# Optimization experiments

Hardware: AMD Instinct MI355X
Metric: run time of the kernel (lower is better)

## Reference

```python
import jax, jax.numpy as jnp
import numpy as np

B, S, D, H, KP, DK = 4, 2048, 1024, 16, 8, 3
DD = D // H
NEG = -1.0e9


def dense(x, W, b):
    return x @ W + b


def dw_conv_causal(x, w, b):
    # x: [B,S,D], w: [DK,D] per-channel kernel, b: [D]; left pad DK-1 zeros -> VALID conv
    xp = jnp.pad(x, ((0, 0), (DK - 1, 0), (0, 0)))
    y = b
    for t in range(DK):
        y = y + xp[:, t:t + S, :] * w[t]
    return y


def split_heads(x):
    return x.reshape(B, S, H, DD).transpose(0, 2, 1, 3)  # [B,H,S,DD]


def pool_causal(x):
    # left pad KP-1 zeros along seq, avg_pool window=stride=KP, VALID
    xp = jnp.pad(x, ((0, 0), (0, 0), (KP - 1, 0), (0, 0)))
    n = (S - 1) // KP + 1  # TF VALID output length
    return xp[:, :, :n * KP, :].reshape(B, H, n, KP, DD).mean(axis=3)


def forward(q, k, v, Wq, bq, Wk, bk, Wv, bv, Wup, bup, Wc, bc,
            wcq, bcq, wck, bck, wcv, bcv):
    norm = float(DD) ** -0.25
    qh = dense(q, Wq, bq) * norm
    kh = dense(k, Wk, bk) * norm
    vh = dense(v, Wv, bv)
    q_in = split_heads(dw_conv_causal(qh, wcq, bcq))
    k_in = split_heads(dw_conv_causal(kh, wck, bck))
    v_in = split_heads(dw_conv_causal(vh, wcv, bcv))
    qp = pool_causal(q_in)  # [B,H,n,DD]
    kp = pool_causal(k_in)
    vp = pool_causal(v_in)
    n = qp.shape[2]
    mask = NEG * (1.0 - jnp.tril(jnp.ones((n, n), dtype=qp.dtype)))
    logits = jnp.einsum('bhnd,bhmd->bhnm', qp, kp) + mask
    attn = jax.nn.softmax(logits, axis=-1)
    out = jnp.einsum('bhnm,bhmd->bhnd', attn, vp)  # [B,H,n,DD]
    up = jnp.repeat(out, KP, axis=2)[:, :, :S, :]  # upsample + crop
    up = dense(up, Wup, bup)
    merged = up.transpose(0, 2, 1, 3).reshape(B, S, D)
    return dense(merged, Wc, bc)


def setup_inputs() -> dict:
    key = jax.random.key(0)
    ks = jax.random.split(key, 20)
    w = lambda i, shp: jax.random.normal(ks[i], shp, dtype=jnp.float32) * 0.02
    return {
        'q': jax.random.normal(ks[0], (B, S, D), dtype=jnp.float32),
        'k': jax.random.normal(ks[1], (B, S, D), dtype=jnp.float32),
        'v': jax.random.normal(ks[2], (B, S, D), dtype=jnp.float32),
        'Wq': w(3, (D, D)), 'bq': jnp.zeros((D,), jnp.float32),
        'Wk': w(4, (D, D)), 'bk': jnp.zeros((D,), jnp.float32),
        'Wv': w(5, (D, D)), 'bv': jnp.zeros((D,), jnp.float32),
        'Wup': w(6, (DD, DD)), 'bup': jnp.zeros((DD,), jnp.float32),
        'Wc': w(7, (D, D)), 'bc': jnp.zeros((D,), jnp.float32),
        'wcq': w(8, (DK, D)), 'bcq': jnp.zeros((D,), jnp.float32),
        'wck': w(9, (DK, D)), 'bck': jnp.zeros((D,), jnp.float32),
        'wcv': w(10, (DK, D)), 'bcv': jnp.zeros((D,), jnp.float32),
    }


def reference(q, k, v, Wq, bq, Wk, bk, Wv, bv, Wup, bup, Wc, bc,
              wcq, bcq, wck, bck, wcv, bcv):
    return forward(q, k, v, Wq, bq, Wk, bk, Wv, bv, Wup, bup, Wc, bc,
                   wcq, bcq, wck, bck, wcv, bcv)
```

## Files before the change

### kernel.cpp

```cpp
#include <hip/hip_runtime.h>
#include <cstdint>
#include <cstddef>

#define Bc  4
#define Sc  2048
#define Dc  1024
#define Hc  16
#define DDc 64
#define Nc  256

typedef unsigned short u16;
typedef unsigned int   u32;
typedef __bf16 bf16_t;
typedef bf16_t bf16x8 __attribute__((ext_vector_type(8)));
typedef float  f32x4  __attribute__((ext_vector_type(4)));

__device__ __forceinline__ u16 f2bf(float x) {
    u32 u = __float_as_uint(x);
    return (u16)((u + 0x7FFFu + ((u >> 16) & 1u)) >> 16);
}
__device__ __forceinline__ u32 pack2(float a, float b) {
    return (u32)f2bf(a) | ((u32)f2bf(b) << 16);
}
__device__ __forceinline__ uint2 pack4(float4 x) {
    return make_uint2(pack2(x.x, x.y), pack2(x.z, x.w));
}
__device__ __forceinline__ float bf2f(u16 x) {
    return __uint_as_float((u32)x << 16);
}
__device__ __forceinline__ float4 f4add(float4 a, float4 b) {
    return make_float4(a.x + b.x, a.y + b.y, a.z + b.z, a.w + b.w);
}

__device__ __forceinline__ void gload_lds16(const void* gp, void* lp) {
    __builtin_amdgcn_global_load_lds(
        reinterpret_cast<const __attribute__((address_space(1))) void*>(
            reinterpret_cast<uintptr_t>(gp)),
        reinterpret_cast<__attribute__((address_space(3))) void*>(
            reinterpret_cast<uintptr_t>(lp)),
        16, 0, 0);
}

__global__ __launch_bounds__(256) void cast_wt4_kernel(
    const float* __restrict__ Wq, const float* __restrict__ Wk,
    const float* __restrict__ Wv, const float* __restrict__ Wc,
    u16* __restrict__ Wt4)
{
    __shared__ float T[64][65];
    const int z = blockIdx.z;
    const float* W = (z == 0) ? Wq : (z == 1) ? Wk : (z == 2) ? Wv : Wc;
    u16* Wt = Wt4 + ((size_t)z << 20);
    const int k0 = blockIdx.y * 64, n0 = blockIdx.x * 64;
    const int c = threadIdx.x & 63, r4 = threadIdx.x >> 6;
    #pragma unroll
    for (int i = 0; i < 16; ++i) {
        int r = i * 4 + r4;
        T[r][c] = W[(size_t)(k0 + r) * 1024 + n0 + c];
    }
    __syncthreads();
    #pragma unroll
    for (int i = 0; i < 16; ++i) {
        int r = i * 4 + r4;
        Wt[(size_t)(n0 + r) * 1024 + k0 + c] = f2bf(T[c][r]);
    }
}

__global__ __launch_bounds__(256) void stage_kernel(
    const float* __restrict__ q, const float* __restrict__ k,
    const float* __restrict__ v, u16* __restrict__ R)
{
    int gid = blockIdx.x * 256 + threadIdx.x;
    int c4 = gid & 255, t = (gid >> 8) & 255, b = (gid >> 16) & 3, inp = gid >> 18;
    const float* src = (inp == 0) ? q : (inp == 1) ? k : v;
    const float4* Xb = (const float4*)(src + (size_t)b * Sc * Dc) + c4;
    const float4* Xr = Xb + ((ptrdiff_t)(t << 3) - 1) * 256;

    float4 r[8];
    if (t > 0) {
        #pragma unroll
        for (int i = 0; i < 8; ++i) r[i] = Xr[(ptrdiff_t)i * 256];
    } else {
        r[0] = make_float4(0.f, 0.f, 0.f, 0.f);
        #pragma unroll
        for (int i = 1; i < 8; ++i) r[i] = Xr[(ptrdiff_t)i * 256];
    }

    float4 s8 = f4add(f4add(f4add(r[0], r[1]), f4add(r[2], r[3])),
                      f4add(f4add(r[4], r[5]), f4add(r[6], r[7])));

    size_t s0 = ((size_t)(inp * 3) << 20) + (((u32)(b * 256 + t)) << 10) + c4 * 4;
    *(uint2*)(R + s0 + (1u << 20)) = pack4(r[0]);
    *(uint2*)(R + s0 + (2u << 20)) = pack4(r[1]);
    if (t < 255) *(uint2*)(R + s0 + 1024) = pack4(s8);
    if (t == 0)  *(uint2*)(R + s0) = make_uint2(0u, 0u);
}

__global__ __launch_bounds__(256) void gemm_sec(
    u16* __restrict__ Rall, const u16* __restrict__ Wt4)
{
    __shared__ __align__(16) u16 As[128 * 32];
    __shared__ __align__(16) u16 Bs[128 * 32];

    const int tid  = threadIdx.x;
    const int lane = tid & 63;
    const int wv   = tid >> 6;
    const int z    = blockIdx.z;
    const int inp  = z / 3;
    const int m0   = blockIdx.y * 128;
    const int n0   = blockIdx.x * 128;

    const char* Ab = (const char*)(Rall + ((size_t)z << 20));
    const char* Bb = (const char*)(Wt4 + ((size_t)inp << 20));

    const int wm   = (wv & 1) * 64;
    const int wn   = (wv >> 1) * 64;
    const int mi   = lane & 15;
    const int quad = lane >> 4;

    f32x4 acc[4][4];
    #pragma unroll
    for (int i = 0; i < 4; ++i)
        #pragma unroll
        for (int j = 0; j < 4; ++j)
            acc[i][j] = (f32x4){0.f, 0.f, 0.f, 0.f};

    const int ra0 = tid >> 2, cb = (tid & 3) * 16;
    char* AsB = (char*)As;
    char* BsB = (char*)Bs;

    for (int k0 = 0; k0 < 1024; k0 += 32) {
        const size_t kb = (size_t)k0 * 2;
        gload_lds16(Ab + ((size_t)(m0 + ra0)      << 11) + kb + cb, AsB + wv * 1024);
        gload_lds16(Ab + ((size_t)(m0 + 64 + ra0) << 11) + kb + cb, AsB + 4096 + wv * 1024);
        gload_lds16(Bb + ((size_t)(n0 + ra0)      << 11) + kb + cb, BsB + wv * 1024);
        gload_lds16(Bb + ((size_t)(n0 + 64 + ra0) << 11) + kb + cb, BsB + 4096 + wv * 1024);
        __syncthreads();

        bf16x8 af[4], bfr[4];
        #pragma unroll
        for (int i = 0; i < 4; ++i)
            af[i] = *reinterpret_cast<const bf16x8*>(&As[(wm + i * 16 + mi) * 32 + quad * 8]);
        #pragma unroll
        for (int j = 0; j < 4; ++j)
            bfr[j] = *reinterpret_cast<const bf16x8*>(&Bs[(wn + j * 16 + mi) * 32 + quad * 8]);

        #pragma unroll
        for (int i = 0; i < 4; ++i)
            #pragma unroll
            for (int j = 0; j < 4; ++j)
                acc[i][j] = __builtin_amdgcn_mfma_f32_16x16x32_bf16(af[i], bfr[j], acc[i][j], 0, 0, 0);

        __syncthreads();
    }

    u16* Cs = Rall + ((size_t)z << 20);
    #pragma unroll
    for (int j = 0; j < 4; ++j) {
        const int col = n0 + wn + j * 16 + mi;
        #pragma unroll
        for (int i = 0; i < 4; ++i) {
            const int row = m0 + wm + i * 16 + quad * 4;
            #pragma unroll
            for (int r = 0; r < 4; ++r)
                Cs[(size_t)(row + r) * 1024 + col] = f2bf(acc[i][j][r]);
        }
    }
}

__global__ __launch_bounds__(256) void combine_kernel(
    const u16* __restrict__ Y,
    const float* __restrict__ wcq, const float* __restrict__ wck, const float* __restrict__ wcv,
    const float* __restrict__ bcq, const float* __restrict__ bck, const float* __restrict__ bcv,
    const float* __restrict__ bq,  const float* __restrict__ bk,  const float* __restrict__ bv,
    u16* __restrict__ qb, u16* __restrict__ kb, u16* __restrict__ vt)
{
    int gid = blockIdx.x * 256 + threadIdx.x;
    int c = gid & 1023, t = (gid >> 10) & 255, b = (gid >> 18) & 3, inp = gid >> 20;
    const float* wc = (inp == 0) ? wcq : (inp == 1) ? wck : wcv;
    const float* bconv = (inp == 0) ? bcq : (inp == 1) ? bck : bcv;
    const float* bl = (inp == 0) ? bq : (inp == 1) ? bk : bv;
    const float nrm = (inp == 2) ? 1.0f : 0.35355339059327373f;

    float w0 = wc[c], w1 = wc[1024 + c], w2 = wc[2048 + c];
    float sumw = w0 + w1 + w2, w12 = w1 + w2;

    u32 lo = gid & 0xFFFFFu;
    size_t z0 = (size_t)(inp * 3) << 20;
    float Y0  = bf2f(Y[z0 + lo]);
    float Y1  = bf2f(Y[z0 + (1u << 20) + lo]);
    float Y2  = bf2f(Y[z0 + (2u << 20) + lo]);
    float Y1p = (t > 0) ? bf2f(Y[z0 + (1u << 20) + lo - 1024]) : 0.f;
    float Y2p = (t > 0) ? bf2f(Y[z0 + (2u << 20) + lo - 1024]) : 0.f;

    float data = sumw * Y0 + w12 * (Y1 - Y1p) + w2 * (Y2 - Y2p);

    float cnt = (t == 0) ? 1.f : 8.f;
    float n0  = (t == 0) ? 0.f : ((t == 1) ? 7.f : 8.f);
    float n1  = (t == 0) ? 0.f : 8.f;
    float n2  = (t == 0) ? 1.f : 8.f;
    float val = 0.125f * (cnt * bconv[c] + nrm * (bl[c] * (n0 * w0 + n1 * w1 + n2 * w2) + data));

    int h = c >> 6, d = c & 63;
    int bh = b * 16 + h;
    u16 bfv = f2bf(val);
    if (inp == 0)
        qb[(((size_t)bh * 256 + t) << 6) + d] = bfv;
    else if (inp == 1)
        kb[(((size_t)bh * 256 + t) << 6) + d] = bfv;
    else
        vt[(size_t)bh * 80 * 256 + (size_t)d * 256 + t] = bfv;
}

__global__ __launch_bounds__(256) void vpad_kernel(u16* __restrict__ vt)
{
    const int bh = blockIdx.x;
    const int tid = threadIdx.x;
    const int rr = tid >> 4;
    const int c0 = (tid & 15) * 16;
    u32 fill = (rr == 0) ? 0x3F803F80u : 0u;
    uint4 val = make_uint4(fill, fill, fill, fill);
    uint4* p = (uint4*)(vt + (size_t)bh * 80 * 256 + (size_t)(64 + rr) * 256 + c0);
    p[0] = val;
    p[1] = val;
}

__global__ __launch_bounds__(256) void attn_mfma(
    const u16* __restrict__ qb, const u16* __restrict__ kb,
    const u16* __restrict__ vt, float* __restrict__ ao)
{
    __shared__ __align__(16) u16 Ps[4][64 * 72];
    const int bh   = blockIdx.x;
    const int tid  = threadIdx.x;
    const int wv   = tid >> 6;
    const int lane = tid & 63;
    const int mi   = lane & 15;
    const int quad = lane >> 4;

    const u16* Qb = qb + (((size_t)bh * 256 + wv * 64) << 6);
    const u16* Kb = kb + ((size_t)bh << 14);
    const u16* Vt = vt + (size_t)bh * 80 * 256;
    u16* P = Ps[wv];

    bf16x8 qf[4][2];
    #pragma unroll
    for (int it = 0; it < 4; ++it)
        #pragma unroll
        for (int kc = 0; kc < 2; ++kc)
            qf[it][kc] = *(const bf16x8*)(Qb + ((it * 16 + mi) << 6) + kc * 32 + quad * 8);

    f32x4 o[4][5];
    #pragma unroll
    for (int it = 0; it < 4; ++it)
        #pragma unroll
        for (int jn = 0; jn < 5; ++jn)
            o[it][jn] = (f32x4){0.f, 0.f, 0.f, 0.f};

    for (int kt = 0; kt <= wv; ++kt) {
        bf16x8 kf[4][2];
        #pragma unroll
        for (int jt = 0; jt < 4; ++jt)
            #pragma unroll
            for (int kc = 0; kc < 2; ++kc)
                kf[jt][kc] = *(const bf16x8*)(Kb + ((kt * 64 + jt * 16 + mi) << 6) + kc * 32 + quad * 8);

        f32x4 s[4][4];
        #pragma unroll
        for (int it = 0; it < 4; ++it)
            #pragma unroll
            for (int jt = 0; jt < 4; ++jt)
                s[it][jt] = (f32x4){0.f, 0.f, 0.f, 0.f};
        #pragma unroll
        for (int kc = 0; kc < 2; ++kc)
            #pragma unroll
            for (int it = 0; it < 4; ++it)
                #pragma unroll
                for (int jt = 0; jt < 4; ++jt)
                    s[it][jt] = __builtin_amdgcn_mfma_f32_16x16x32_bf16(qf[it][kc], kf[jt][kc], s[it][jt], 0, 0, 0);

        const bool diag = (kt == wv);
        #pragma unroll
        for (int it = 0; it < 4; ++it)
            #pragma unroll
            for (int jt = 0; jt < 4; ++jt)
                #pragma unroll
                for (int r = 0; r < 4; ++r) {
                    int qrow = it * 16 + quad * 4 + r;
                    int kcol = jt * 16 + mi;
                    float e = __expf(s[it][jt][r]);
                    if (diag && kcol > qrow) e = 0.f;
                    P[qrow * 72 + kcol] = f2bf(e);
                }

        bf16x8 pf[4][2];
        #pragma unroll
        for (int it = 0; it < 4; ++it)
            #pragma unroll
            for (int kc = 0; kc < 2; ++kc)
                pf[it][kc] = *(const bf16x8*)(P + (it * 16 + mi) * 72 + kc * 32 + quad * 8);

        bf16x8 vf[5][2];
        #pragma unroll
        for (int jn = 0; jn < 5; ++jn)
            #pragma unroll
            for (int kc = 0; kc < 2; ++kc)
                vf[jn][kc] = *(const bf16x8*)(Vt + (size_t)(jn * 16 + mi) * 256 + kt * 64 + kc * 32 + quad * 8);

        #pragma unroll
        for (int kc = 0; kc < 2; ++kc)
            #pragma unroll
            for (int it = 0; it < 4; ++it)
                #pragma unroll
                for (int jn = 0; jn < 5; ++jn)
                    o[it][jn] = __builtin_amdgcn_mfma_f32_16x16x32_bf16(pf[it][kc], vf[jn][kc], o[it][jn], 0, 0, 0);
    }

    #pragma unroll
    for (int it = 0; it < 4; ++it) {
        float inv[4];
        #pragma unroll
        for (int r = 0; r < 4; ++r) {
            float lv = __shfl(o[it][4][r], (lane & 48));
            inv[r] = 1.0f / lv;
        }
        #pragma unroll
        for (int jn = 0; jn < 4; ++jn)
            #pragma unroll
            for (int r = 0; r < 4; ++r) {
                int row = wv * 64 + it * 16 + quad * 4 + r;
                ao[(((size_t)bh * 256 + row) << 6) + jn * 16 + mi] = o[it][jn][r] * inv[r];
            }
    }
}

__global__ __launch_bounds__(256) void updense_kernel(
    const float* __restrict__ ao, const float* __restrict__ Wup,
    const float* __restrict__ bup, u16* __restrict__ ms)
{
    __shared__ float Ws[64 * 64];
    __shared__ float rows[4 * 64];
    const int tid = threadIdx.x;

    #pragma unroll
    for (int i = 0; i < 4; ++i)
        ((float4*)Ws)[tid + 256 * i] = ((const float4*)Wup)[tid + 256 * i];
    rows[tid] = ao[(size_t)blockIdx.x * 256 + tid];
    __syncthreads();

    const int r = tid >> 6, dp = tid & 63;
    const int R = blockIdx.x * 4 + r;
    const int b = R >> 12;
    const int h = (R >> 8) & 15;
    const int m = R & 255;

    float acc = bup[dp];
    #pragma unroll
    for (int d = 0; d < 64; ++d)
        acc += rows[r * 64 + d] * Ws[d * 64 + dp];

    ms[((size_t)(b * Nc + m) << 10) + h * 64 + dp] = f2bf(acc);
}

__global__ __launch_bounds__(256) void gemm_out(
    const u16* __restrict__ A, const u16* __restrict__ Bt,
    const float* __restrict__ bias, float* __restrict__ C)
{
    __shared__ __align__(16) u16 As[64 * 32];
    __shared__ __align__(16) u16 Bs[64 * 32];

    const int tid  = threadIdx.x;
    const int lane = tid & 63;
    const int wv   = tid >> 6;
    const int m0   = blockIdx.y * 64;
    const int n0   = blockIdx.x * 64;

    const int wm   = (wv >> 1) * 32;
    const int wn   = (wv & 1) * 32;
    const int mi   = lane & 15;
    const int quad = lane >> 4;

    f32x4 acc[2][2];
    #pragma unroll
    for (int i = 0; i < 2; ++i)
        #pragma unroll
        for (int j = 0; j < 2; ++j)
            acc[i][j] = (f32x4){0.f, 0.f, 0.f, 0.f};

    const char* Ab = (const char*)A;
    const char* Bb = (const char*)Bt;
    const int ra0 = tid >> 2, cb = (tid & 3) * 16;
    char* AsB = (char*)As;
    char* BsB = (char*)Bs;

    for (int k0 = 0; k0 < 1024; k0 += 32) {
        const size_t kb = (size_t)k0 * 2;
        gload_lds16(Ab + ((size_t)(m0 + ra0) << 11) + kb + cb, AsB + wv * 1024);
        gload_lds16(Bb + ((size_t)(n0 + ra0) << 11) + kb + cb, BsB + wv * 1024);
        __syncthreads();

        bf16x8 af[2], bfr[2];
        #pragma unroll
        for (int i = 0; i < 2; ++i)
            af[i] = *reinterpret_cast<const bf16x8*>(&As[(wm + i * 16 + mi) * 32 + quad * 8]);
        #pragma unroll
        for (int j = 0; j < 2; ++j)
            bfr[j] = *reinterpret_cast<const bf16x8*>(&Bs[(wn + j * 16 + mi) * 32 + quad * 8]);

        #pragma unroll
        for (int i = 0; i < 2; ++i)
            #pragma unroll
            for (int j = 0; j < 2; ++j)
                acc[i][j] = __builtin_amdgcn_mfma_f32_16x16x32_bf16(af[i], bfr[j], acc[i][j], 0, 0, 0);

        __syncthreads();
    }

    #pragma unroll
    for (int j = 0; j < 2; ++j) {
        const int col = n0 + wn + j * 16 + mi;
        const float bv = bias[col];
        #pragma unroll
        for (int i = 0; i < 2; ++i) {
            const int row = m0 + wm + i * 16 + quad * 4;
            #pragma unroll
            for (int r = 0; r < 4; ++r)
                C[(size_t)(row + r) * 1024 + col] = acc[i][j][r] + bv;
        }
    }
}

__global__ __launch_bounds__(256) void upsample_kernel(
    const float* __restrict__ C, float* __restrict__ out)
{
    const float4* C4  = (const float4*)C;
    float4*       out4 = (float4*)out;
    int idx0 = blockIdx.x * 1024 + threadIdx.x;
    #pragma unroll
    for (int rep = 0; rep < 4; ++rep) {
        int o4   = idx0 + rep * 256;
        int col4 = o4 & 255;
        int rowo = o4 >> 8;
        int b    = rowo >> 11;
        int tc   = (rowo & 2047) >> 3;
        out4[o4] = C4[(size_t)((b << 8) + tc) * 256 + col4];
    }
}

extern "C" void kernel_launch(void* const* d_in, const int* in_sizes, int n_in,
                              void* d_out, int out_size, void* d_ws, size_t ws_size,
                              hipStream_t stream) {
    const float* q   = (const float*)d_in[0];
    const float* k   = (const float*)d_in[1];
    const float* v   = (const float*)d_in[2];
    const float* Wq  = (const float*)d_in[3];
    const float* bq  = (const float*)d_in[4];
    const float* Wk  = (const float*)d_in[5];
    const float* bk  = (const float*)d_in[6];
    const float* Wv  = (const float*)d_in[7];
    const float* bv  = (const float*)d_in[8];
    const float* Wup = (const float*)d_in[9];
    const float* bup = (const float*)d_in[10];
    const float* Wc  = (const float*)d_in[11];
    const float* bc  = (const float*)d_in[12];
    const float* wcq = (const float*)d_in[13];
    const float* bcq = (const float*)d_in[14];
    const float* wck = (const float*)d_in[15];
    const float* bck = (const float*)d_in[16];
    const float* wcv = (const float*)d_in[17];
    const float* bcv = (const float*)d_in[18];

    u16* Rall = (u16*)d_out;

    char* wsb = (char*)d_ws;
    u16*   Wt4 = (u16*)wsb;
    u16*   qb  = (u16*)(wsb + 8388608);
    u16*   kb  = (u16*)(wsb + 10485760);
    u16*   vt  = (u16*)(wsb + 12582912);
    float* ao  = (float*)(wsb + 15204352);
    u16*   ms  = (u16*)(wsb + 19398656);
    float* Cf  = ao;

    cast_wt4_kernel<<<dim3(16, 16, 4), 256, 0, stream>>>(Wq, Wk, Wv, Wc, Wt4);
    stage_kernel<<<3072, 256, 0, stream>>>(q, k, v, Rall);
    gemm_sec<<<dim3(8, 8, 9), 256, 0, stream>>>(Rall, Wt4);
    combine_kernel<<<12288, 256, 0, stream>>>(Rall, wcq, wck, wcv, bcq, bck, bcv,
                                              bq, bk, bv, qb, kb, vt);
    vpad_kernel<<<64, 256, 0, stream>>>(vt);
    attn_mfma<<<64, 256, 0, stream>>>(qb, kb, vt, ao);
    updense_kernel<<<(Bc * Hc * Nc) / 4, 256, 0, stream>>>(ao, Wup, bup, ms);
    gemm_out<<<dim3(16, 16), 256, 0, stream>>>(ms, Wt4 + ((size_t)3 << 20), bc, Cf);
    upsample_kernel<<<2048, 256, 0, stream>>>(Cf, (float*)d_out);
}
```

Baseline: 276.4 us.

## Fold depthwise conv into QKV weights and fuse combine into K=3072 GEMM

Folds the causal depthwise-conv weights and the pooling scale into three scaled copies of each projection weight, so that one GEMM with K=3072 over staged pooled-sum and difference features produces pooled q/k/v directly. Bias terms are precomputed per position class. This replaces the nine separate GEMMs and the elementwise combine kernel, whose bf16 round trip through memory is removed. The attention kernel is also split into one 64-thread block per query tile instead of four waves per block, which raises block count but leaves causal tiles imbalanced across blocks. Staging reads ten rows per output instead of eight, and the larger weight workspace adds traffic in the prep kernel.

```diff
diff --git a/kernel.cpp b/kernel.cpp
--- a/kernel.cpp
+++ b/kernel.cpp
@@ -30,6 +30,9 @@
 }
 __device__ __forceinline__ float4 f4add(float4 a, float4 b) {
     return make_float4(a.x + b.x, a.y + b.y, a.z + b.z, a.w + b.w);
+}
+__device__ __forceinline__ float4 f4sub(float4 a, float4 b) {
+    return make_float4(a.x - b.x, a.y - b.y, a.z - b.z, a.w - b.w);
 }
 
 __device__ __forceinline__ void gload_lds16(const void* gp, void* lp) {
@@ -41,15 +44,16 @@
         16, 0, 0);
 }
 
-__global__ __launch_bounds__(256) void cast_wt4_kernel(
+__global__ __launch_bounds__(256) void prep_wt3(
     const float* __restrict__ Wq, const float* __restrict__ Wk,
     const float* __restrict__ Wv, const float* __restrict__ Wc,
-    u16* __restrict__ Wt4)
+    const float* __restrict__ wcq, const float* __restrict__ wck,
+    const float* __restrict__ wcv,
+    u16* __restrict__ Wt3, u16* __restrict__ Wtc)
 {
     __shared__ float T[64][65];
     const int z = blockIdx.z;
     const float* W = (z == 0) ? Wq : (z == 1) ? Wk : (z == 2) ? Wv : Wc;
-    u16* Wt = Wt4 + ((size_t)z << 20);
     const int k0 = blockIdx.y * 64, n0 = blockIdx.x * 64;
     const int c = threadIdx.x & 63, r4 = threadIdx.x >> 6;
     #pragma unroll
@@ -58,68 +62,112 @@
         T[r][c] = W[(size_t)(k0 + r) * 1024 + n0 + c];
     }
     __syncthreads();
-    #pragma unroll
-    for (int i = 0; i < 16; ++i) {
-        int r = i * 4 + r4;
-        Wt[(size_t)(n0 + r) * 1024 + k0 + c] = f2bf(T[c][r]);
-    }
+    if (z < 3) {
+        const float* wc = (z == 0) ? wcq : (z == 1) ? wck : wcv;
+        const float fs = 0.125f * ((z == 2) ? 1.0f : 0.35355339059327373f);
+        u16* dst0 = Wt3 + (size_t)z * 3145728;
+        #pragma unroll
+        for (int i = 0; i < 16; ++i) {
+            int r = i * 4 + r4;
+            int n = n0 + r;
+            float w0 = wc[n], w1 = wc[1024 + n], w2 = wc[2048 + n];
+            float s2 = fs * w2, s1 = s2 + fs * w1, s0 = s1 + fs * w0;
+            float x = T[c][r];
+            u16* dst = dst0 + (size_t)n * 3072 + k0 + c;
+            dst[0]    = f2bf(x * s0);
+            dst[1024] = f2bf(x * s1);
+            dst[2048] = f2bf(x * s2);
+        }
+    } else {
+        #pragma unroll
+        for (int i = 0; i < 16; ++i) {
+            int r = i * 4 + r4;
+            Wtc[(size_t)(n0 + r) * 1024 + k0 + c] = f2bf(T[c][r]);
+        }
+    }
+}
+
+__global__ __launch_bounds__(256) void prep_bias(
+    const float* __restrict__ wcq, const float* __restrict__ wck, const float* __restrict__ wcv,
+    const float* __restrict__ bcq, const float* __restrict__ bck, const float* __restrict__ bcv,
+    const float* __restrict__ bq,  const float* __restrict__ bk,  const float* __restrict__ bv,
+    float* __restrict__ biasT)
+{
+    int gid = blockIdx.x * 256 + threadIdx.x;
+    int c = gid & 1023, z = gid >> 10;
+    const float* wc    = (z == 0) ? wcq : (z == 1) ? wck : wcv;
+    const float* bconv = (z == 0) ? bcq : (z == 1) ? bck : bcv;
+    const float* bl    = (z == 0) ? bq  : (z == 1) ? bk  : bv;
+    const float nrm = (z == 2) ? 1.0f : 0.35355339059327373f;
+    float w0 = wc[c], w1 = wc[1024 + c], w2 = wc[2048 + c];
+    float bc_ = bconv[c], bl_ = bl[c];
+    float* dst = biasT + (size_t)z * 3072 + c;
+    dst[0]    = 0.125f * (bc_ + nrm * bl_ * w2);
+    dst[1024] = 0.125f * (8.f * bc_ + nrm * bl_ * (7.f * w0 + 8.f * w1 + 8.f * w2));
+    dst[2048] = 0.125f * (8.f * bc_ + nrm * bl_ * 8.f * (w0 + w1 + w2));
 }
 
 __global__ __launch_bounds__(256) void stage_kernel(
     const float* __restrict__ q, const float* __restrict__ k,
-    const float* __restrict__ v, u16* __restrict__ R)
+    const float* __restrict__ v, u16* __restrict__ A3)
 {
     int gid = blockIdx.x * 256 + threadIdx.x;
     int c4 = gid & 255, t = (gid >> 8) & 255, b = (gid >> 16) & 3, inp = gid >> 18;
     const float* src = (inp == 0) ? q : (inp == 1) ? k : v;
     const float4* Xb = (const float4*)(src + (size_t)b * Sc * Dc) + c4;
-    const float4* Xr = Xb + ((ptrdiff_t)(t << 3) - 1) * 256;
-
-    float4 r[8];
-    if (t > 0) {
-        #pragma unroll
-        for (int i = 0; i < 8; ++i) r[i] = Xr[(ptrdiff_t)i * 256];
+    const float4* Xr = Xb + ((ptrdiff_t)(t << 3) - 9) * 256;
+
+    float4 r[10];
+    if (t >= 2) {
+        #pragma unroll
+        for (int i = 0; i < 10; ++i) r[i] = Xr[(ptrdiff_t)i * 256];
+    } else if (t == 1) {
+        r[0] = make_float4(0.f, 0.f, 0.f, 0.f);
+        #pragma unroll
+        for (int i = 1; i < 10; ++i) r[i] = Xr[(ptrdiff_t)i * 256];
     } else {
-        r[0] = make_float4(0.f, 0.f, 0.f, 0.f);
-        #pragma unroll
-        for (int i = 1; i < 8; ++i) r[i] = Xr[(ptrdiff_t)i * 256];
-    }
-
-    float4 s8 = f4add(f4add(f4add(r[0], r[1]), f4add(r[2], r[3])),
+        #pragma unroll
+        for (int i = 0; i < 9; ++i) r[i] = make_float4(0.f, 0.f, 0.f, 0.f);
+        r[9] = Xr[(ptrdiff_t)9 * 256];
+    }
+
+    float4 A0 = f4add(f4add(f4add(r[0], r[1]), f4add(r[2], r[3])),
                       f4add(f4add(r[4], r[5]), f4add(r[6], r[7])));
-
-    size_t s0 = ((size_t)(inp * 3) << 20) + (((u32)(b * 256 + t)) << 10) + c4 * 4;
-    *(uint2*)(R + s0 + (1u << 20)) = pack4(r[0]);
-    *(uint2*)(R + s0 + (2u << 20)) = pack4(r[1]);
-    if (t < 255) *(uint2*)(R + s0 + 1024) = pack4(s8);
-    if (t == 0)  *(uint2*)(R + s0) = make_uint2(0u, 0u);
-}
-
-__global__ __launch_bounds__(256) void gemm_sec(
-    u16* __restrict__ Rall, const u16* __restrict__ Wt4)
-{
-    __shared__ __align__(16) u16 As[128 * 32];
+    float4 B1 = f4sub(r[8], r[0]);
+    float4 B2 = f4sub(r[9], r[1]);
+
+    size_t s0 = (size_t)inp * 3145728 + (size_t)(b * 256 + t) * 3072 + c4 * 4;
+    *(uint2*)(A3 + s0)        = pack4(A0);
+    *(uint2*)(A3 + s0 + 1024) = pack4(B1);
+    *(uint2*)(A3 + s0 + 2048) = pack4(B2);
+}
+
+__global__ __launch_bounds__(256) void gemm_qkv(
+    const u16* __restrict__ A3, const u16* __restrict__ Wt3,
+    const float* __restrict__ biasT,
+    u16* __restrict__ qb, u16* __restrict__ kb, u16* __restrict__ vt)
+{
+    __shared__ __align__(16) u16 As[64 * 32];
     __shared__ __align__(16) u16 Bs[128 * 32];
 
     const int tid  = threadIdx.x;
     const int lane = tid & 63;
     const int wv   = tid >> 6;
     const int z    = blockIdx.z;
-    const int inp  = z / 3;
-    const int m0   = blockIdx.y * 128;
+    const int m0   = blockIdx.y * 64;
     const int n0   = blockIdx.x * 128;
 
-    const char* Ab = (const char*)(Rall + ((size_t)z << 20));
-    const char* Bb = (const char*)(Wt4 + ((size_t)inp << 20));
-
-    const int wm   = (wv & 1) * 64;
+    const int wm   = (wv & 1) * 32;
     const int wn   = (wv >> 1) * 64;
     const int mi   = lane & 15;
     const int quad = lane >> 4;
 
-    f32x4 acc[4][4];
-    #pragma unroll
-    for (int i = 0; i < 4; ++i)
+    const char* Ab = (const char*)(A3  + (size_t)z * 3145728);
+    const char* Bb = (const char*)(Wt3 + (size_t)z * 3145728);
+
+    f32x4 acc[2][4];
+    #pragma unroll
+    for (int i = 0; i < 2; ++i)
         #pragma unroll
         for (int j = 0; j < 4; ++j)
             acc[i][j] = (f32x4){0.f, 0.f, 0.f, 0.f};
@@ -128,24 +176,23 @@
     char* AsB = (char*)As;
     char* BsB = (char*)Bs;
 
-    for (int k0 = 0; k0 < 1024; k0 += 32) {
+    for (int k0 = 0; k0 < 3072; k0 += 32) {
         const size_t kb = (size_t)k0 * 2;
-        gload_lds16(Ab + ((size_t)(m0 + ra0)      << 11) + kb + cb, AsB + wv * 1024);
-        gload_lds16(Ab + ((size_t)(m0 + 64 + ra0) << 11) + kb + cb, AsB + 4096 + wv * 1024);
-        gload_lds16(Bb + ((size_t)(n0 + ra0)      << 11) + kb + cb, BsB + wv * 1024);
-        gload_lds16(Bb + ((size_t)(n0 + 64 + ra0) << 11) + kb + cb, BsB + 4096 + wv * 1024);
+        gload_lds16(Ab + (size_t)(m0 + ra0)      * 6144 + kb + cb, AsB + wv * 1024);
+        gload_lds16(Bb + (size_t)(n0 + ra0)      * 6144 + kb + cb, BsB + wv * 1024);
+        gload_lds16(Bb + (size_t)(n0 + 64 + ra0) * 6144 + kb + cb, BsB + 4096 + wv * 1024);
         __syncthreads();
 
-        bf16x8 af[4], bfr[4];
-        #pragma unroll
-        for (int i = 0; i < 4; ++i)
+        bf16x8 af[2], bfr[4];
+        #pragma unroll
+        for (int i = 0; i < 2; ++i)
             af[i] = *reinterpret_cast<const bf16x8*>(&As[(wm + i * 16 + mi) * 32 + quad * 8]);
         #pragma unroll
         for (int j = 0; j < 4; ++j)
             bfr[j] = *reinterpret_cast<const bf16x8*>(&Bs[(wn + j * 16 + mi) * 32 + quad * 8]);
 
         #pragma unroll
-        for (int i = 0; i < 4; ++i)
+        for (int i = 0; i < 2; ++i)
             #pragma unroll
             for (int j = 0; j < 4; ++j)
                 acc[i][j] = __builtin_amdgcn_mfma_f32_16x16x32_bf16(af[i], bfr[j], acc[i][j], 0, 0, 0);
@@ -153,62 +200,47 @@
         __syncthreads();
     }
 
-    u16* Cs = Rall + ((size_t)z << 20);
-    #pragma unroll
-    for (int j = 0; j < 4; ++j) {
-        const int col = n0 + wn + j * 16 + mi;
-        #pragma unroll
-        for (int i = 0; i < 4; ++i) {
-            const int row = m0 + wm + i * 16 + quad * 4;
-            #pragma unroll
-            for (int r = 0; r < 4; ++r)
-                Cs[(size_t)(row + r) * 1024 + col] = f2bf(acc[i][j][r]);
+    const float* bT = biasT + (size_t)z * 3072;
+    if (z == 2) {
+        #pragma unroll
+        for (int j = 0; j < 4; ++j) {
+            const int col = n0 + wn + j * 16 + mi;
+            const int h = col >> 6, d = col & 63;
+            #pragma unroll
+            for (int i = 0; i < 2; ++i) {
+                const int row = m0 + wm + i * 16 + quad * 4;
+                const int b = row >> 8, t0 = row & 255;
+                const int bh = b * 16 + h;
+                u16 w[4];
+                #pragma unroll
+                for (int r = 0; r < 4; ++r) {
+                    int t = t0 + r;
+                    w[r] = f2bf(acc[i][j][r] + bT[(t < 2 ? t : 2) * 1024 + col]);
+                }
+                *(uint2*)(vt + (size_t)bh * 20480 + (size_t)d * 256 + t0) =
+                    make_uint2((u32)w[0] | ((u32)w[1] << 16), (u32)w[2] | ((u32)w[3] << 16));
+            }
         }
-    }
-}
-
-__global__ __launch_bounds__(256) void combine_kernel(
-    const u16* __restrict__ Y,
-    const float* __restrict__ wcq, const float* __restrict__ wck, const float* __restrict__ wcv,
-    const float* __restrict__ bcq, const float* __restrict__ bck, const float* __restrict__ bcv,
-    const float* __restrict__ bq,  const float* __restrict__ bk,  const float* __restrict__ bv,
-    u16* __restrict__ qb, u16* __restrict__ kb, u16* __restrict__ vt)
-{
-    int gid = blockIdx.x * 256 + threadIdx.x;
-    int c = gid & 1023, t = (gid >> 10) & 255, b = (gid >> 18) & 3, inp = gid >> 20;
-    const float* wc = (inp == 0) ? wcq : (inp == 1) ? wck : wcv;
-    const float* bconv = (inp == 0) ? bcq : (inp == 1) ? bck : bcv;
-    const float* bl = (inp == 0) ? bq : (inp == 1) ? bk : bv;
-    const float nrm = (inp == 2) ? 1.0f : 0.35355339059327373f;
-
-    float w0 = wc[c], w1 = wc[1024 + c], w2 = wc[2048 + c];
-    float sumw = w0 + w1 + w2, w12 = w1 + w2;
-
-    u32 lo = gid & 0xFFFFFu;
-    size_t z0 = (size_t)(inp * 3) << 20;
-    float Y0  = bf2f(Y[z0 + lo]);
-    float Y1  = bf2f(Y[z0 + (1u << 20) + lo]);
-    float Y2  = bf2f(Y[z0 + (2u << 20) + lo]);
-    float Y1p = (t > 0) ? bf2f(Y[z0 + (1u << 20) + lo - 1024]) : 0.f;
-    float Y2p = (t > 0) ? bf2f(Y[z0 + (2u << 20) + lo - 1024]) : 0.f;
-
-    float data = sumw * Y0 + w12 * (Y1 - Y1p) + w2 * (Y2 - Y2p);
-
-    float cnt = (t == 0) ? 1.f : 8.f;
-    float n0  = (t == 0) ? 0.f : ((t == 1) ? 7.f : 8.f);
-    float n1  = (t == 0) ? 0.f : 8.f;
-    float n2  = (t == 0) ? 1.f : 8.f;
-    float val = 0.125f * (cnt * bconv[c] + nrm * (bl[c] * (n0 * w0 + n1 * w1 + n2 * w2) + data));
-
-    int h = c >> 6, d = c & 63;
-    int bh = b * 16 + h;
-    u16 bfv = f2bf(val);
-    if (inp == 0)
-        qb[(((size_t)bh * 256 + t) << 6) + d] = bfv;
-    else if (inp == 1)
-        kb[(((size_t)bh * 256 + t) << 6) + d] = bfv;
-    else
-        vt[(size_t)bh * 80 * 256 + (size_t)d * 256 + t] = bfv;
+    } else {
+        u16* dst = z ? kb : qb;
+        #pragma unroll
+        for (int j = 0; j < 4; ++j) {
+            const int col = n0 + wn + j * 16 + mi;
+            const int h = col >> 6, d = col & 63;
+            #pragma unroll
+            for (int i = 0; i < 2; ++i) {
+                const int row = m0 + wm + i * 16 + quad * 4;
+                const int b = row >> 8;
+                const int bh = b * 16 + h;
+                #pragma unroll
+                for (int r = 0; r < 4; ++r) {
+                    int t = (row & 255) + r;
+                    dst[(((size_t)bh * 256 + t) << 6) + d] =
+                        f2bf(acc[i][j][r] + bT[(t < 2 ? t : 2) * 1024 + col]);
+                }
+            }
+        }
+    }
 }
 
 __global__ __launch_bounds__(256) void vpad_kernel(u16* __restrict__ vt)
@@ -224,22 +256,20 @@
     p[1] = val;
 }
 
-__global__ __launch_bounds__(256) void attn_mfma(
+__global__ __launch_bounds__(64) void attn_mfma(
     const u16* __restrict__ qb, const u16* __restrict__ kb,
     const u16* __restrict__ vt, float* __restrict__ ao)
 {
-    __shared__ __align__(16) u16 Ps[4][64 * 72];
-    const int bh   = blockIdx.x;
-    const int tid  = threadIdx.x;
-    const int wv   = tid >> 6;
-    const int lane = tid & 63;
+    __shared__ __align__(16) u16 P[64 * 72];
+    const int qt   = blockIdx.x;
+    const int bh   = blockIdx.y;
+    const int lane = threadIdx.x;
     const int mi   = lane & 15;
     const int quad = lane >> 4;
 
-    const u16* Qb = qb + (((size_t)bh * 256 + wv * 64) << 6);
+    const u16* Qb = qb + (((size_t)bh * 256 + qt * 64) << 6);
     const u16* Kb = kb + ((size_t)bh << 14);
     const u16* Vt = vt + (size_t)bh * 80 * 256;
-    u16* P = Ps[wv];
 
     bf16x8 qf[4][2];
     #pragma unroll
@@ -255,7 +285,7 @@
         for (int jn = 0; jn < 5; ++jn)
             o[it][jn] = (f32x4){0.f, 0.f, 0.f, 0.f};
 
-    for (int kt = 0; kt <= wv; ++kt) {
+    for (int kt = 0; kt <= qt; ++kt) {
         bf16x8 kf[4][2];
         #pragma unroll
         for (int jt = 0; jt < 4; ++jt)
@@ -277,7 +307,7 @@
                 for (int jt = 0; jt < 4; ++jt)
                     s[it][jt] = __builtin_amdgcn_mfma_f32_16x16x32_bf16(qf[it][kc], kf[jt][kc], s[it][jt], 0, 0, 0);
 
-        const bool diag = (kt == wv);
+        const bool diag = (kt == qt);
         #pragma unroll
         for (int it = 0; it < 4; ++it)
             #pragma unroll
@@ -326,7 +356,7 @@
         for (int jn = 0; jn < 4; ++jn)
             #pragma unroll
             for (int r = 0; r < 4; ++r) {
-                int row = wv * 64 + it * 16 + quad * 4 + r;
+                int row = qt * 64 + it * 16 + quad * 4 + r;
                 ao[(((size_t)bh * 256 + row) << 6) + jn * 16 + mi] = o[it][jn][r] * inv[r];
             }
     }
@@ -468,25 +498,26 @@
     const float* wcv = (const float*)d_in[17];
     const float* bcv = (const float*)d_in[18];
 
-    u16* Rall = (u16*)d_out;
+    u16* A3 = (u16*)d_out;
 
     char* wsb = (char*)d_ws;
-    u16*   Wt4 = (u16*)wsb;
-    u16*   qb  = (u16*)(wsb + 8388608);
-    u16*   kb  = (u16*)(wsb + 10485760);
-    u16*   vt  = (u16*)(wsb + 12582912);
-    float* ao  = (float*)(wsb + 15204352);
-    u16*   ms  = (u16*)(wsb + 19398656);
-    float* Cf  = ao;
-
-    cast_wt4_kernel<<<dim3(16, 16, 4), 256, 0, stream>>>(Wq, Wk, Wv, Wc, Wt4);
-    stage_kernel<<<3072, 256, 0, stream>>>(q, k, v, Rall);
-    gemm_sec<<<dim3(8, 8, 9), 256, 0, stream>>>(Rall, Wt4);
-    combine_kernel<<<12288, 256, 0, stream>>>(Rall, wcq, wck, wcv, bcq, bck, bcv,
-                                              bq, bk, bv, qb, kb, vt);
+    u16*   Wt3   = (u16*)wsb;
+    u16*   Wtc   = (u16*)(wsb + 18874368);
+    float* biasT = (float*)(wsb + 20971520);
+    u16*   qb    = (u16*)(wsb + 21008384);
+    u16*   kb    = (u16*)(wsb + 23105536);
+    u16*   vt    = (u16*)(wsb + 25202688);
+    float* ao    = (float*)(wsb + 27824128);
+    u16*   ms    = (u16*)(wsb + 32018432);
+    float* Cf    = ao;
+
+    prep_wt3<<<dim3(16, 16, 4), 256, 0, stream>>>(Wq, Wk, Wv, Wc, wcq, wck, wcv, Wt3, Wtc);
+    prep_bias<<<12, 256, 0, stream>>>(wcq, wck, wcv, bcq, bck, bcv, bq, bk, bv, biasT);
+    stage_kernel<<<3072, 256, 0, stream>>>(q, k, v, A3);
+    gemm_qkv<<<dim3(8, 16, 3), 256, 0, stream>>>(A3, Wt3, biasT, qb, kb, vt);
     vpad_kernel<<<64, 256, 0, stream>>>(vt);
-    attn_mfma<<<64, 256, 0, stream>>>(qb, kb, vt, ao);
+    attn_mfma<<<dim3(4, 64), 64, 0, stream>>>(qb, kb, vt, ao);
     updense_kernel<<<(Bc * Hc * Nc) / 4, 256, 0, stream>>>(ao, Wup, bup, ms);
-    gemm_out<<<dim3(16, 16), 256, 0, stream>>>(ms, Wt4 + ((size_t)3 << 20), bc, Cf);
+    gemm_out<<<dim3(16, 16), 256, 0, stream>>>(ms, Wtc, bc, Cf);
     upsample_kernel<<<2048, 256, 0, stream>>>(Cf, (float*)d_out);
 }
```

Result: no change. 281.1 us (+1.7%).
